# Optimization experiments

Hardware: AMD Instinct MI355X
Metric: run time of the kernel (lower is better)

Reference implementation:

```python
import jax, jax.numpy as jnp
import numpy as np

B = 262144
EDGES_SRC = np.array([0, 0, 0, 0])
EDGES_DST = np.array([1, 2, 3, 4])
PRED_IDS = np.array([[0, 10, 14], [1, 11, 18], [2, 12, 22], [3, 13, 26]])
O_IDS = np.array([0, 1, 2, 3, 10, 11, 12, 13, 14, 18, 22, 26])


def _xavier(k, shape):
    fan_out, fan_in = shape
    bound = float(np.sqrt(6.0 / (fan_in + fan_out)))
    return jax.random.uniform(k, shape, jnp.float32, -bound, bound)


def setup_inputs() -> dict:
    key = jax.random.key(0)
    ks = jax.random.split(key, 12)
    return {
        "initial_c": jax.random.uniform(ks[0], (B, 30), jnp.float32),
        "initial_s": jax.random.normal(ks[1], (B, 9), jnp.float32),
        "current_c": jax.random.uniform(ks[2], (B, 30), jnp.float32),
        "eps": jax.random.normal(ks[3], (B, 8), jnp.float32),
        # GnnMessagePassing params (torch Linear: y = x @ W.T + b)
        "W1": _xavier(ks[4], (128, 13)), "b1": jnp.zeros(128, jnp.float32),
        "W2": _xavier(ks[5], (39, 128)), "b2": jnp.zeros(39, jnp.float32),
        "W3": _xavier(ks[6], (128, 39)), "b3": jnp.zeros(128, jnp.float32),
        "Wm": _xavier(ks[7], (8, 128)), "bm": jnp.zeros(8, jnp.float32),
        "Wv": _xavier(ks[8], (8, 128)), "bv": jnp.zeros(8, jnp.float32),
        # Decoder params: [25 -> 32 -> 12], sigmoid output (binary=True)
        "Wd1": _xavier(ks[9], (32, 25)), "bd1": jnp.zeros(32, jnp.float32),
        "Wd2": _xavier(ks[10], (12, 32)), "bd2": jnp.zeros(12, jnp.float32),
    }


def reference(initial_c, initial_s, current_c, eps,
              W1, b1, W2, b2, W3, b3, Wm, bm, Wv, bv, Wd1, bd1, Wd2, bd2):
    bsz = current_c.shape[0]
    eye = jnp.eye(5, dtype=current_c.dtype)
    # per-edge constant one-hot pair features: [4, 10]
    edge_onehot = jnp.concatenate([eye[EDGES_SRC], eye[EDGES_DST]], axis=-1)
    edge_onehot = jnp.broadcast_to(edge_onehot[:, None, :], (4, bsz, 10))
    # gather predicate triplets per edge: [B, 4, 3] -> [4, B, 3]
    preds = jnp.transpose(current_c[:, PRED_IDS], (1, 0, 2))
    inp_mp = jnp.concatenate([edge_onehot, preds], axis=-1)  # [4, B, 13]

    # message MLP + sum over edge dim
    x = jax.nn.relu(jnp.einsum('ebi,oi->ebo', inp_mp, W1) + b1)  # [4, B, 128]
    x = jax.nn.relu(jnp.einsum('ebi,oi->ebo', x, W2) + b2)       # [4, B, 39]
    x = x.sum(axis=0)                                            # [B, 39]
    x = jax.nn.relu(x @ W3.T + b3)                               # [B, 128]
    means = x @ Wm.T + bm                                        # [B, 8]
    log_var = x @ Wv.T + bv                                      # [B, 8]

    # reparameterization
    z = eps * jnp.exp(0.5 * log_var) + means

    # decoder: [one-hot(node 0) | initial_c[o_ids] | z] -> sigmoid MLP
    node0 = jnp.broadcast_to(eye[0], (bsz, 5))
    inp_dec = jnp.concatenate([node0, initial_c[:, O_IDS], z], axis=1)  # [B, 25]
    h = jax.nn.relu(inp_dec @ Wd1.T + bd1)
    recon_x = jax.nn.sigmoid(h @ Wd2.T + bd2)  # [B, 12]
    return recon_x, means, log_var, z
```

## Files before the change

kernel.cpp:

```cpp
#include <hip/hip_runtime.h>
#include <hip/hip_bf16.h>

#define TPB 256
#define PREP_BLOCKS 64

typedef __attribute__((ext_vector_type(8))) short short8;
typedef __attribute__((ext_vector_type(4))) float f32x4;

#define G_W2F   0
#define G_MVF   12288
#define G_D1F   16384
#define G_D2F   18432
#define G_CEAB  19456
#define G_B2P   23552
#define G_B3    23744
#define G_BMV   24256
#define G_D1C   24320
#define G_BD2   24448
#define G_W3F   24512
#define G_END   40896

#define PW_SWC  0
#define PW_SIC  768
#define PW_ST   2048
#define PW_BUF  4352
#define PW_MH   8704
#define PW_SZ   9984
#define LDS_TOT (4 * PW_SZ)

__device__ __forceinline__ unsigned short f2bf(float f) {
    unsigned int u = __float_as_uint(f);
    unsigned int r = u + 0x7fffu + ((u >> 16) & 1u);
    return (unsigned short)(r >> 16);
}
__device__ __forceinline__ unsigned int pk(float a, float b) {
    __hip_bfloat162 h = __float22bfloat162_rn(make_float2(a, b));
    unsigned int u; __builtin_memcpy(&u, &h, 4); return u;
}
__device__ __forceinline__ unsigned short bfbits(float v) {
    return (unsigned short)(pk(v, v) & 0xffffu);
}

__global__ void prep_kernel(
    const float* __restrict__ W1, const float* __restrict__ b1,
    const float* __restrict__ W2, const float* __restrict__ b2,
    const float* __restrict__ W3, const float* __restrict__ b3,
    const float* __restrict__ Wm, const float* __restrict__ bm,
    const float* __restrict__ Wv, const float* __restrict__ bv,
    const float* __restrict__ Wd1, const float* __restrict__ bd1,
    const float* __restrict__ Wd2, const float* __restrict__ bd2,
    unsigned char* __restrict__ ws)
{
    const int g0 = blockIdx.x * TPB + threadIdx.x;
    const int gs = gridDim.x * TPB;
    unsigned short* w2f = (unsigned short*)(ws + G_W2F);
    for (int i = g0; i < 6144; i += gs) {
        int j = i & 7, lane = (i >> 3) & 63, ts = i >> 9;
        int tt = ts >> 2, s = ts & 3;
        int n = 16 * tt + (lane & 15), k = 32 * s + 8 * (lane >> 4) + j;
        w2f[i] = (n < 39) ? f2bf(W2[n * 128 + k]) : 0;
    }
    unsigned short* w3f = (unsigned short*)(ws + G_W3F);
    for (int i = g0; i < 8192; i += gs) {
        int j = i & 7, lane = (i >> 3) & 63, ns = i >> 9;
        int nt = ns >> 1, s = ns & 1;
        int n = 16 * nt + (lane & 15), k = 32 * s + 8 * (lane >> 4) + j;
        w3f[i] = (k < 39) ? f2bf(W3[n * 39 + k]) : 0;
    }
    unsigned short* mvf = (unsigned short*)(ws + G_MVF);
    for (int i = g0; i < 2048; i += gs) {
        int j = i & 7, lane = (i >> 3) & 63, s = i >> 9;
        int n = lane & 15, k = 32 * s + 8 * (lane >> 4) + j;
        mvf[i] = f2bf(n < 8 ? Wm[n * 128 + k] : Wv[(n - 8) * 128 + k]);
    }
    unsigned short* d1f = (unsigned short*)(ws + G_D1F);
    for (int i = g0; i < 1024; i += gs) {
        int j = i & 7, lane = (i >> 3) & 63, tt = i >> 9;
        int n = 16 * tt + (lane & 15), k = 8 * (lane >> 4) + j;
        d1f[i] = (k < 20) ? f2bf(Wd1[n * 25 + 5 + k]) : 0;
    }
    unsigned short* d2f = (unsigned short*)(ws + G_D2F);
    for (int i = g0; i < 512; i += gs) {
        int j = i & 7, lane = i >> 3;
        int n = lane & 15, k = 8 * (lane >> 4) + j;
        d2f[i] = (n < 12) ? f2bf(Wd2[n * 32 + k]) : 0;
    }
    unsigned short* ceab = (unsigned short*)(ws + G_CEAB);
    for (int i = g0; i < 2048; i += gs) {
        int c = i & 3, n = (i >> 2) & 127, e = i >> 9;
        float v = (c < 3) ? W1[n * 13 + 10 + c]
                          : (W1[n * 13 + 0] + W1[n * 13 + 6 + e] + b1[n]);
        ceab[i] = f2bf(v);
    }
    float* fb = (float*)(ws + G_B2P);
    for (int i = g0; i < 48; i += gs) fb[i] = (i < 39) ? b2[i] : 0.f;
    fb = (float*)(ws + G_B3);
    for (int i = g0; i < 128; i += gs) fb[i] = b3[i];
    fb = (float*)(ws + G_BMV);
    for (int i = g0; i < 16; i += gs) fb[i] = (i < 8) ? bm[i] : bv[i - 8];
    fb = (float*)(ws + G_D1C);
    for (int i = g0; i < 32; i += gs) fb[i] = Wd1[i * 25 + 0] + bd1[i];
    fb = (float*)(ws + G_BD2);
    for (int i = g0; i < 16; i += gs) fb[i] = (i < 12) ? bd2[i] : 0.f;
}

union S8 { short8 v; uint4 u; };

__global__ __launch_bounds__(TPB, 2) void vae_mfma(
    const float* __restrict__ ic, const float* __restrict__ cc,
    const float* __restrict__ eps,
    const unsigned char* __restrict__ ws,
    float* __restrict__ out, int B)
{
    __shared__ __attribute__((aligned(16))) unsigned char lds[LDS_TOT];
    const int tid = threadIdx.x;

    const int lane = tid & 63, w = tid >> 6;
    const int quad = lane >> 4, n16 = lane & 15;
    const bool q0 = (quad == 0);
    const long rb = ((long)blockIdx.x * 4 + w) * 16;
    unsigned char* pw = lds + w * PW_SZ;

    {
        int r = lane >> 2, g = lane & 3;
        long R = rb + r;
        const int cbase[4] = {0, 2, 10, 12};
        const int csing[4] = {14, 18, 22, 26};
        const float* crow = cc + R * 30;
        const float* irow = ic + R * 30;
        float2 cp = *(const float2*)(crow + cbase[g]);
        float  cs = crow[csing[g]];
        float2 ip = *(const float2*)(irow + cbase[g]);
        float  is = irow[csing[g]];
        float* swc = (float*)(pw + PW_SWC);
        *(float2*)(swc + r * 12 + 2 * g) = cp;
        swc[r * 12 + 8 + g] = cs;
        unsigned short* sic = (unsigned short*)(pw + PW_SIC);
        *(unsigned int*)(sic + r * 40 + 2 * g) = pk(ip.x, ip.y);
        sic[r * 40 + 8 + g] = bfbits(is);
        if (g < 3) *(unsigned long long*)(sic + r * 40 + 20 + 4 * g) = 0ull;
        unsigned short* st = (unsigned short*)(pw + PW_ST);
        *(unsigned long long*)(st + r * 72 + 48 + 4 * g) = 0ull;
    }

    short8 B2[12];
    #pragma unroll
    for (int ts = 0; ts < 12; ts++) {
        S8 x; x.u = *(const uint4*)(ws + G_W2F + (ts * 64 + lane) * 16);
        B2[ts] = x.v;
    }
    const float b2v0 = *(const float*)(ws + G_B2P + n16 * 4);
    const float b2v1 = *(const float*)(ws + G_B2P + (16 + n16) * 4);
    const float b2v2 = *(const float*)(ws + G_B2P + (32 + n16) * 4);

    float pa[4], pb[4], pc[4];
    {
        const float* swcr = (const float*)(pw + PW_SWC) + n16 * 12;
        float4 t0 = *(const float4*)(swcr);
        float4 t1 = *(const float4*)(swcr + 4);
        float4 t2 = *(const float4*)(swcr + 8);
        pa[0] = t0.x; pa[1] = t0.y; pa[2] = t0.z; pa[3] = t0.w;
        pb[0] = t1.x; pb[1] = t1.y; pb[2] = t1.z; pb[3] = t1.w;
        pc[0] = t2.x; pc[1] = t2.y; pc[2] = t2.z; pc[3] = t2.w;
    }

    f32x4 ss0 = {0,0,0,0}, ss1 = {0,0,0,0}, ss2 = {0,0,0,0};
    unsigned short* x1t = (unsigned short*)(pw + PW_BUF);

    #pragma unroll
    for (int e = 0; e < 4; e++) {
        S8 a1;
        a1.u.x = q0 ? pk(pa[e], pb[e]) : 0u;
        a1.u.y = q0 ? pk(pc[e], 1.0f) : 0u;
        a1.u.z = 0u; a1.u.w = 0u;
        const unsigned long long* cb =
            (const unsigned long long*)(ws + G_CEAB + e * 1024);
        f32x4 cr[8];
        #pragma unroll
        for (int nt = 0; nt < 8; nt++) {
            unsigned long long bw = cb[nt * 16 + n16];
            S8 bf;
            bf.u.x = q0 ? (unsigned int)bw : 0u;
            bf.u.y = q0 ? (unsigned int)(bw >> 32) : 0u;
            bf.u.z = 0u; bf.u.w = 0u;
            f32x4 z = {0, 0, 0, 0};
            cr[nt] = __builtin_amdgcn_mfma_f32_16x16x32_bf16(a1.v, bf.v, z, 0, 0, 0);
        }
        #pragma unroll
        for (int nt = 0; nt < 8; nt++) {
            #pragma unroll
            for (int r = 0; r < 4; r++)
                x1t[(quad * 4 + r) * 136 + nt * 16 + n16] = bfbits(fmaxf(cr[nt][r], 0.f));
        }
        f32x4 c0 = {b2v0, b2v0, b2v0, b2v0};
        f32x4 c1 = {b2v1, b2v1, b2v1, b2v1};
        f32x4 c2 = {b2v2, b2v2, b2v2, b2v2};
        #pragma unroll
        for (int s = 0; s < 4; s++) {
            S8 a2; a2.u = *(const uint4*)(x1t + n16 * 136 + s * 32 + quad * 8);
            c0 = __builtin_amdgcn_mfma_f32_16x16x32_bf16(a2.v, B2[s],     c0, 0, 0, 0);
            c1 = __builtin_amdgcn_mfma_f32_16x16x32_bf16(a2.v, B2[4 + s], c1, 0, 0, 0);
            c2 = __builtin_amdgcn_mfma_f32_16x16x32_bf16(a2.v, B2[8 + s], c2, 0, 0, 0);
        }
        #pragma unroll
        for (int r = 0; r < 4; r++) {
            ss0[r] += fmaxf(c0[r], 0.f);
            ss1[r] += fmaxf(c1[r], 0.f);
            ss2[r] += fmaxf(c2[r], 0.f);
        }
    }

    unsigned short* st = (unsigned short*)(pw + PW_ST);
    #pragma unroll
    for (int r = 0; r < 4; r++) {
        int row = quad * 4 + r;
        st[row * 72 + n16]      = bfbits(ss0[r]);
        st[row * 72 + 16 + n16] = bfbits(ss1[r]);
        st[row * 72 + 32 + n16] = bfbits(ss2[r]);
    }

    S8 A30, A31;
    A30.u = *(const uint4*)(st + n16 * 72 + quad * 8);
    A31.u = *(const uint4*)(st + n16 * 72 + 32 + quad * 8);
    const uint4* w3g = (const uint4*)(ws + G_W3F);
    unsigned short* x3t = (unsigned short*)(pw + PW_BUF);
    const float* b3p = (const float*)(ws + G_B3);
    #pragma unroll
    for (int nt = 0; nt < 8; nt++) {
        float bb = b3p[nt * 16 + n16];
        f32x4 c = {bb, bb, bb, bb};
        S8 bf0, bf1;
        bf0.u = w3g[(nt * 2 + 0) * 64 + lane];
        bf1.u = w3g[(nt * 2 + 1) * 64 + lane];
        c = __builtin_amdgcn_mfma_f32_16x16x32_bf16(A30.v, bf0.v, c, 0, 0, 0);
        c = __builtin_amdgcn_mfma_f32_16x16x32_bf16(A31.v, bf1.v, c, 0, 0, 0);
        #pragma unroll
        for (int r = 0; r < 4; r++)
            x3t[(quad * 4 + r) * 136 + nt * 16 + n16] = bfbits(fmaxf(c[r], 0.f));
    }

    S8 Ah0, Ah1, Ah2, Ah3;
    Ah0.u = *(const uint4*)(x3t + n16 * 136 + 0  + quad * 8);
    Ah1.u = *(const uint4*)(x3t + n16 * 136 + 32 + quad * 8);
    Ah2.u = *(const uint4*)(x3t + n16 * 136 + 64 + quad * 8);
    Ah3.u = *(const uint4*)(x3t + n16 * 136 + 96 + quad * 8);
    float bmvv = *(const float*)(ws + G_BMV + n16 * 4);
    f32x4 cm = {bmvv, bmvv, bmvv, bmvv};
    {
        S8 bm0; bm0.u = *(const uint4*)(ws + G_MVF + (0 * 64 + lane) * 16);
        cm = __builtin_amdgcn_mfma_f32_16x16x32_bf16(Ah0.v, bm0.v, cm, 0, 0, 0);
        S8 bm1; bm1.u = *(const uint4*)(ws + G_MVF + (1 * 64 + lane) * 16);
        cm = __builtin_amdgcn_mfma_f32_16x16x32_bf16(Ah1.v, bm1.v, cm, 0, 0, 0);
        S8 bm2; bm2.u = *(const uint4*)(ws + G_MVF + (2 * 64 + lane) * 16);
        cm = __builtin_amdgcn_mfma_f32_16x16x32_bf16(Ah2.v, bm2.v, cm, 0, 0, 0);
        S8 bm3; bm3.u = *(const uint4*)(ws + G_MVF + (3 * 64 + lane) * 16);
        cm = __builtin_amdgcn_mfma_f32_16x16x32_bf16(Ah3.v, bm3.v, cm, 0, 0, 0);
    }
    float* mlv = (float*)(pw + PW_MH);
    #pragma unroll
    for (int r = 0; r < 4; r++) mlv[(quad * 4 + r) * 18 + n16] = cm[r];

    {
        int r = lane >> 2, g = lane & 3;
        long R = rb + r;
        const float* mrow = mlv + r * 18;
        float2 mn = *(const float2*)(mrow + 2 * g);
        float2 lv = *(const float2*)(mrow + 8 + 2 * g);
        float2 ev = *(const float2*)(eps + R * 8 + 2 * g);
        float z0 = fmaf(ev.x, __expf(0.5f * lv.x), mn.x);
        float z1 = fmaf(ev.y, __expf(0.5f * lv.y), mn.y);
        *(float2*)(out + (long)B * 12 + R * 8 + 2 * g) = mn;
        *(float2*)(out + (long)B * 20 + R * 8 + 2 * g) = lv;
        *(float2*)(out + (long)B * 28 + R * 8 + 2 * g) = make_float2(z0, z1);
        unsigned short* sic = (unsigned short*)(pw + PW_SIC);
        *(unsigned int*)(sic + r * 40 + 12 + 2 * g) = pk(z0, z1);
    }

    S8 Ad;
    Ad.u = *(const uint4*)((const unsigned short*)(pw + PW_SIC) + n16 * 40 + quad * 8);
    unsigned short* ht = (unsigned short*)(pw + PW_MH);
    #pragma unroll
    for (int t = 0; t < 2; t++) {
        float dc = *(const float*)(ws + G_D1C + (t * 16 + n16) * 4);
        f32x4 c = {dc, dc, dc, dc};
        S8 bd; bd.u = *(const uint4*)(ws + G_D1F + (t * 64 + lane) * 16);
        c = __builtin_amdgcn_mfma_f32_16x16x32_bf16(Ad.v, bd.v, c, 0, 0, 0);
        #pragma unroll
        for (int r = 0; r < 4; r++)
            ht[(quad * 4 + r) * 40 + t * 16 + n16] = bfbits(fmaxf(c[r], 0.f));
    }

    S8 Ah2d; Ah2d.u = *(const uint4*)(ht + n16 * 40 + quad * 8);
    float bd2v = *(const float*)(ws + G_BD2 + n16 * 4);
    f32x4 cr2 = {bd2v, bd2v, bd2v, bd2v};
    S8 b2d; b2d.u = *(const uint4*)(ws + G_D2F + lane * 16);
    cr2 = __builtin_amdgcn_mfma_f32_16x16x32_bf16(Ah2d.v, b2d.v, cr2, 0, 0, 0);
    if (n16 < 12) {
        #pragma unroll
        for (int r = 0; r < 4; r++)
            out[(rb + quad * 4 + r) * 12 + n16] = 1.f / (1.f + __expf(-cr2[r]));
    }
}

extern "C" void kernel_launch(void* const* d_in, const int* in_sizes, int n_in,
                              void* d_out, int out_size, void* d_ws, size_t ws_size,
                              hipStream_t stream) {
    const float* ic  = (const float*)d_in[0];
    const float* cc  = (const float*)d_in[2];
    const float* eps = (const float*)d_in[3];

    const int B = in_sizes[3] / 8;
    const int nblocks = B / 64;

    prep_kernel<<<PREP_BLOCKS, TPB, 0, stream>>>(
        (const float*)d_in[4],  (const float*)d_in[5],
        (const float*)d_in[6],  (const float*)d_in[7],
        (const float*)d_in[8],  (const float*)d_in[9],
        (const float*)d_in[10], (const float*)d_in[11],
        (const float*)d_in[12], (const float*)d_in[13],
        (const float*)d_in[14], (const float*)d_in[15],
        (const float*)d_in[16], (const float*)d_in[17],
        (unsigned char*)d_ws);
    vae_mfma<<<nblocks, TPB, 0, stream>>>(
        ic, cc, eps, (const unsigned char*)d_ws, (float*)d_out, B);
}
```

Before: 191.8 us.

## Chain MFMA layers in registers via transposed products and permuted weight K order

Swaps operand roles so each layer computes the transposed product, with weights as A and activations as B. Weight K indices are permuted in the prep kernel so one layer's accumulator output feeds the next layer's B fragment directly in registers. This removes all LDS staging, LDS round trips and the shared memory allocation. Lane exchanges for log_var and z use ds_bpermute, and outputs are written as float4 per lane. The risk is more register pressure and a fragile permutation mapping.

```diff
diff --git a/kernel.cpp b/kernel.cpp
--- a/kernel.cpp
+++ b/kernel.cpp
@@ -20,14 +20,6 @@
 #define G_W3F   24512
 #define G_END   40896
 
-#define PW_SWC  0
-#define PW_SIC  768
-#define PW_ST   2048
-#define PW_BUF  4352
-#define PW_MH   8704
-#define PW_SZ   9984
-#define LDS_TOT (4 * PW_SZ)
-
 __device__ __forceinline__ unsigned short f2bf(float f) {
     unsigned int u = __float_as_uint(f);
     unsigned int r = u + 0x7fffu + ((u >> 16) & 1u);
@@ -36,9 +28,6 @@
 __device__ __forceinline__ unsigned int pk(float a, float b) {
     __hip_bfloat162 h = __float22bfloat162_rn(make_float2(a, b));
     unsigned int u; __builtin_memcpy(&u, &h, 4); return u;
-}
-__device__ __forceinline__ unsigned short bfbits(float v) {
-    return (unsigned short)(pk(v, v) & 0xffffu);
 }
 
 __global__ void prep_kernel(
@@ -56,34 +45,39 @@
     unsigned short* w2f = (unsigned short*)(ws + G_W2F);
     for (int i = g0; i < 6144; i += gs) {
         int j = i & 7, lane = (i >> 3) & 63, ts = i >> 9;
-        int tt = ts >> 2, s = ts & 3;
-        int n = 16 * tt + (lane & 15), k = 32 * s + 8 * (lane >> 4) + j;
-        w2f[i] = (n < 39) ? f2bf(W2[n * 128 + k]) : 0;
+        int t = ts >> 2, s = ts & 3, q = lane >> 4;
+        int n = 16 * t + (lane & 15);
+        int phys = 16 * (2 * s + (j >> 2)) + 4 * q + (j & 3);
+        w2f[i] = (n < 39) ? f2bf(W2[n * 128 + phys]) : 0;
     }
     unsigned short* w3f = (unsigned short*)(ws + G_W3F);
     for (int i = g0; i < 8192; i += gs) {
         int j = i & 7, lane = (i >> 3) & 63, ns = i >> 9;
-        int nt = ns >> 1, s = ns & 1;
-        int n = 16 * nt + (lane & 15), k = 32 * s + 8 * (lane >> 4) + j;
-        w3f[i] = (k < 39) ? f2bf(W3[n * 39 + k]) : 0;
+        int nt = ns >> 1, s = ns & 1, q = lane >> 4;
+        int n = 16 * nt + (lane & 15);
+        int phys = 16 * (2 * s + (j >> 2)) + 4 * q + (j & 3);
+        w3f[i] = (phys < 39) ? f2bf(W3[n * 39 + phys]) : 0;
     }
     unsigned short* mvf = (unsigned short*)(ws + G_MVF);
     for (int i = g0; i < 2048; i += gs) {
         int j = i & 7, lane = (i >> 3) & 63, s = i >> 9;
-        int n = lane & 15, k = 32 * s + 8 * (lane >> 4) + j;
-        mvf[i] = f2bf(n < 8 ? Wm[n * 128 + k] : Wv[(n - 8) * 128 + k]);
+        int q = lane >> 4, n = lane & 15;
+        int phys = 16 * (2 * s + (j >> 2)) + 4 * q + (j & 3);
+        mvf[i] = f2bf(n < 8 ? Wm[n * 128 + phys] : Wv[(n - 8) * 128 + phys]);
     }
     unsigned short* d1f = (unsigned short*)(ws + G_D1F);
     for (int i = g0; i < 1024; i += gs) {
         int j = i & 7, lane = (i >> 3) & 63, tt = i >> 9;
-        int n = 16 * tt + (lane & 15), k = 8 * (lane >> 4) + j;
-        d1f[i] = (k < 20) ? f2bf(Wd1[n * 25 + 5 + k]) : 0;
+        int q = lane >> 4, n = 16 * tt + (lane & 15);
+        int phys = 16 * (j >> 2) + 4 * q + (j & 3);
+        d1f[i] = (phys < 20) ? f2bf(Wd1[n * 25 + 5 + phys]) : 0;
     }
     unsigned short* d2f = (unsigned short*)(ws + G_D2F);
     for (int i = g0; i < 512; i += gs) {
         int j = i & 7, lane = i >> 3;
-        int n = lane & 15, k = 8 * (lane >> 4) + j;
-        d2f[i] = (n < 12) ? f2bf(Wd2[n * 32 + k]) : 0;
+        int q = lane >> 4, n = lane & 15;
+        int phys = 16 * (j >> 2) + 4 * q + (j & 3);
+        d2f[i] = (n < 12) ? f2bf(Wd2[n * 32 + phys]) : 0;
     }
     unsigned short* ceab = (unsigned short*)(ws + G_CEAB);
     for (int i = g0; i < 2048; i += gs) {
@@ -106,101 +100,74 @@
 
 union S8 { short8 v; uint4 u; };
 
+#define MFMA(a, b, c) __builtin_amdgcn_mfma_f32_16x16x32_bf16(a, b, c, 0, 0, 0)
+
 __global__ __launch_bounds__(TPB, 2) void vae_mfma(
     const float* __restrict__ ic, const float* __restrict__ cc,
     const float* __restrict__ eps,
     const unsigned char* __restrict__ ws,
     float* __restrict__ out, int B)
 {
-    __shared__ __attribute__((aligned(16))) unsigned char lds[LDS_TOT];
     const int tid = threadIdx.x;
-
     const int lane = tid & 63, w = tid >> 6;
     const int quad = lane >> 4, n16 = lane & 15;
     const bool q0 = (quad == 0);
     const long rb = ((long)blockIdx.x * 4 + w) * 16;
-    unsigned char* pw = lds + w * PW_SZ;
-
-    {
-        int r = lane >> 2, g = lane & 3;
-        long R = rb + r;
-        const int cbase[4] = {0, 2, 10, 12};
-        const int csing[4] = {14, 18, 22, 26};
-        const float* crow = cc + R * 30;
-        const float* irow = ic + R * 30;
-        float2 cp = *(const float2*)(crow + cbase[g]);
-        float  cs = crow[csing[g]];
-        float2 ip = *(const float2*)(irow + cbase[g]);
-        float  is = irow[csing[g]];
-        float* swc = (float*)(pw + PW_SWC);
-        *(float2*)(swc + r * 12 + 2 * g) = cp;
-        swc[r * 12 + 8 + g] = cs;
-        unsigned short* sic = (unsigned short*)(pw + PW_SIC);
-        *(unsigned int*)(sic + r * 40 + 2 * g) = pk(ip.x, ip.y);
-        sic[r * 40 + 8 + g] = bfbits(is);
-        if (g < 3) *(unsigned long long*)(sic + r * 40 + 20 + 4 * g) = 0ull;
-        unsigned short* st = (unsigned short*)(pw + PW_ST);
-        *(unsigned long long*)(st + r * 72 + 48 + 4 * g) = 0ull;
-    }
-
-    short8 B2[12];
-    #pragma unroll
-    for (int ts = 0; ts < 12; ts++) {
-        S8 x; x.u = *(const uint4*)(ws + G_W2F + (ts * 64 + lane) * 16);
-        B2[ts] = x.v;
-    }
-    const float b2v0 = *(const float*)(ws + G_B2P + n16 * 4);
-    const float b2v1 = *(const float*)(ws + G_B2P + (16 + n16) * 4);
-    const float b2v2 = *(const float*)(ws + G_B2P + (32 + n16) * 4);
-
-    float pa[4], pb[4], pc[4];
-    {
-        const float* swcr = (const float*)(pw + PW_SWC) + n16 * 12;
-        float4 t0 = *(const float4*)(swcr);
-        float4 t1 = *(const float4*)(swcr + 4);
-        float4 t2 = *(const float4*)(swcr + 8);
-        pa[0] = t0.x; pa[1] = t0.y; pa[2] = t0.z; pa[3] = t0.w;
-        pb[0] = t1.x; pb[1] = t1.y; pb[2] = t1.z; pb[3] = t1.w;
-        pc[0] = t2.x; pc[1] = t2.y; pc[2] = t2.z; pc[3] = t2.w;
-    }
+    const long Rl = rb + n16;
+
+    float pa[4] = {0,0,0,0}, pb[4] = {0,0,0,0}, pc[4] = {0,0,0,0};
+    if (q0) {
+        const float* crow = cc + Rl * 30;
+        float2 t0 = *(const float2*)(crow);
+        float2 t1 = *(const float2*)(crow + 2);
+        float2 t2 = *(const float2*)(crow + 10);
+        float2 t3 = *(const float2*)(crow + 12);
+        pa[0] = t0.x; pa[1] = t0.y; pa[2] = t1.x; pa[3] = t1.y;
+        pb[0] = t2.x; pb[1] = t2.y; pb[2] = t3.x; pb[3] = t3.y;
+        pc[0] = crow[14]; pc[1] = crow[18]; pc[2] = crow[22]; pc[3] = crow[26];
+    }
+
+    S8 W2F[12];
+    #pragma unroll
+    for (int ts = 0; ts < 12; ts++)
+        W2F[ts].u = *(const uint4*)(ws + G_W2F + (ts * 64 + lane) * 16);
+    const float* b2p = (const float*)(ws + G_B2P);
+    f32x4 b2q[3];
+    #pragma unroll
+    for (int t = 0; t < 3; t++)
+        b2q[t] = *(const f32x4*)(b2p + 16 * t + 4 * quad);
 
     f32x4 ss0 = {0,0,0,0}, ss1 = {0,0,0,0}, ss2 = {0,0,0,0};
-    unsigned short* x1t = (unsigned short*)(pw + PW_BUF);
 
     #pragma unroll
     for (int e = 0; e < 4; e++) {
-        S8 a1;
-        a1.u.x = q0 ? pk(pa[e], pb[e]) : 0u;
-        a1.u.y = q0 ? pk(pc[e], 1.0f) : 0u;
-        a1.u.z = 0u; a1.u.w = 0u;
+        S8 bp;
+        bp.u.x = q0 ? pk(pa[e], pb[e]) : 0u;
+        bp.u.y = q0 ? pk(pc[e], 1.0f) : 0u;
+        bp.u.z = 0u; bp.u.w = 0u;
         const unsigned long long* cb =
             (const unsigned long long*)(ws + G_CEAB + e * 1024);
-        f32x4 cr[8];
+        S8 xf[4];
         #pragma unroll
-        for (int nt = 0; nt < 8; nt++) {
-            unsigned long long bw = cb[nt * 16 + n16];
-            S8 bf;
-            bf.u.x = q0 ? (unsigned int)bw : 0u;
-            bf.u.y = q0 ? (unsigned int)(bw >> 32) : 0u;
-            bf.u.z = 0u; bf.u.w = 0u;
-            f32x4 z = {0, 0, 0, 0};
-            cr[nt] = __builtin_amdgcn_mfma_f32_16x16x32_bf16(a1.v, bf.v, z, 0, 0, 0);
+        for (int mt = 0; mt < 8; mt++) {
+            unsigned long long bw = cb[mt * 16 + n16];
+            S8 af;
+            af.u.x = q0 ? (unsigned int)bw : 0u;
+            af.u.y = q0 ? (unsigned int)(bw >> 32) : 0u;
+            af.u.z = 0u; af.u.w = 0u;
+            f32x4 z4 = {0,0,0,0};
+            f32x4 cr = MFMA(af.v, bp.v, z4);
+            unsigned int lo = pk(fmaxf(cr[0], 0.f), fmaxf(cr[1], 0.f));
+            unsigned int hi = pk(fmaxf(cr[2], 0.f), fmaxf(cr[3], 0.f));
+            if ((mt & 1) == 0) { xf[mt >> 1].u.x = lo; xf[mt >> 1].u.y = hi; }
+            else               { xf[mt >> 1].u.z = lo; xf[mt >> 1].u.w = hi; }
         }
-        #pragma unroll
-        for (int nt = 0; nt < 8; nt++) {
-            #pragma unroll
-            for (int r = 0; r < 4; r++)
-                x1t[(quad * 4 + r) * 136 + nt * 16 + n16] = bfbits(fmaxf(cr[nt][r], 0.f));
-        }
-        f32x4 c0 = {b2v0, b2v0, b2v0, b2v0};
-        f32x4 c1 = {b2v1, b2v1, b2v1, b2v1};
-        f32x4 c2 = {b2v2, b2v2, b2v2, b2v2};
+        f32x4 c0 = b2q[0], c1 = b2q[1], c2 = b2q[2];
         #pragma unroll
         for (int s = 0; s < 4; s++) {
-            S8 a2; a2.u = *(const uint4*)(x1t + n16 * 136 + s * 32 + quad * 8);
-            c0 = __builtin_amdgcn_mfma_f32_16x16x32_bf16(a2.v, B2[s],     c0, 0, 0, 0);
-            c1 = __builtin_amdgcn_mfma_f32_16x16x32_bf16(a2.v, B2[4 + s], c1, 0, 0, 0);
-            c2 = __builtin_amdgcn_mfma_f32_16x16x32_bf16(a2.v, B2[8 + s], c2, 0, 0, 0);
+            c0 = MFMA(W2F[s].v,     xf[s].v, c0);
+            c1 = MFMA(W2F[4 + s].v, xf[s].v, c1);
+            c2 = MFMA(W2F[8 + s].v, xf[s].v, c2);
         }
         #pragma unroll
         for (int r = 0; r < 4; r++) {
@@ -210,95 +177,100 @@
         }
     }
 
-    unsigned short* st = (unsigned short*)(pw + PW_ST);
-    #pragma unroll
-    for (int r = 0; r < 4; r++) {
-        int row = quad * 4 + r;
-        st[row * 72 + n16]      = bfbits(ss0[r]);
-        st[row * 72 + 16 + n16] = bfbits(ss1[r]);
-        st[row * 72 + 32 + n16] = bfbits(ss2[r]);
-    }
-
-    S8 A30, A31;
-    A30.u = *(const uint4*)(st + n16 * 72 + quad * 8);
-    A31.u = *(const uint4*)(st + n16 * 72 + 32 + quad * 8);
+    S8 sf0, sf1;
+    sf0.u.x = pk(ss0[0], ss0[1]); sf0.u.y = pk(ss0[2], ss0[3]);
+    sf0.u.z = pk(ss1[0], ss1[1]); sf0.u.w = pk(ss1[2], ss1[3]);
+    sf1.u.x = pk(ss2[0], ss2[1]); sf1.u.y = pk(ss2[2], ss2[3]);
+    sf1.u.z = 0u; sf1.u.w = 0u;
+
     const uint4* w3g = (const uint4*)(ws + G_W3F);
-    unsigned short* x3t = (unsigned short*)(pw + PW_BUF);
     const float* b3p = (const float*)(ws + G_B3);
+    S8 hf[4];
     #pragma unroll
     for (int nt = 0; nt < 8; nt++) {
-        float bb = b3p[nt * 16 + n16];
-        f32x4 c = {bb, bb, bb, bb};
-        S8 bf0, bf1;
-        bf0.u = w3g[(nt * 2 + 0) * 64 + lane];
-        bf1.u = w3g[(nt * 2 + 1) * 64 + lane];
-        c = __builtin_amdgcn_mfma_f32_16x16x32_bf16(A30.v, bf0.v, c, 0, 0, 0);
-        c = __builtin_amdgcn_mfma_f32_16x16x32_bf16(A31.v, bf1.v, c, 0, 0, 0);
-        #pragma unroll
-        for (int r = 0; r < 4; r++)
-            x3t[(quad * 4 + r) * 136 + nt * 16 + n16] = bfbits(fmaxf(c[r], 0.f));
-    }
-
-    S8 Ah0, Ah1, Ah2, Ah3;
-    Ah0.u = *(const uint4*)(x3t + n16 * 136 + 0  + quad * 8);
-    Ah1.u = *(const uint4*)(x3t + n16 * 136 + 32 + quad * 8);
-    Ah2.u = *(const uint4*)(x3t + n16 * 136 + 64 + quad * 8);
-    Ah3.u = *(const uint4*)(x3t + n16 * 136 + 96 + quad * 8);
-    float bmvv = *(const float*)(ws + G_BMV + n16 * 4);
-    f32x4 cm = {bmvv, bmvv, bmvv, bmvv};
-    {
-        S8 bm0; bm0.u = *(const uint4*)(ws + G_MVF + (0 * 64 + lane) * 16);
-        cm = __builtin_amdgcn_mfma_f32_16x16x32_bf16(Ah0.v, bm0.v, cm, 0, 0, 0);
-        S8 bm1; bm1.u = *(const uint4*)(ws + G_MVF + (1 * 64 + lane) * 16);
-        cm = __builtin_amdgcn_mfma_f32_16x16x32_bf16(Ah1.v, bm1.v, cm, 0, 0, 0);
-        S8 bm2; bm2.u = *(const uint4*)(ws + G_MVF + (2 * 64 + lane) * 16);
-        cm = __builtin_amdgcn_mfma_f32_16x16x32_bf16(Ah2.v, bm2.v, cm, 0, 0, 0);
-        S8 bm3; bm3.u = *(const uint4*)(ws + G_MVF + (3 * 64 + lane) * 16);
-        cm = __builtin_amdgcn_mfma_f32_16x16x32_bf16(Ah3.v, bm3.v, cm, 0, 0, 0);
-    }
-    float* mlv = (float*)(pw + PW_MH);
-    #pragma unroll
-    for (int r = 0; r < 4; r++) mlv[(quad * 4 + r) * 18 + n16] = cm[r];
-
-    {
-        int r = lane >> 2, g = lane & 3;
-        long R = rb + r;
-        const float* mrow = mlv + r * 18;
-        float2 mn = *(const float2*)(mrow + 2 * g);
-        float2 lv = *(const float2*)(mrow + 8 + 2 * g);
-        float2 ev = *(const float2*)(eps + R * 8 + 2 * g);
-        float z0 = fmaf(ev.x, __expf(0.5f * lv.x), mn.x);
-        float z1 = fmaf(ev.y, __expf(0.5f * lv.y), mn.y);
-        *(float2*)(out + (long)B * 12 + R * 8 + 2 * g) = mn;
-        *(float2*)(out + (long)B * 20 + R * 8 + 2 * g) = lv;
-        *(float2*)(out + (long)B * 28 + R * 8 + 2 * g) = make_float2(z0, z1);
-        unsigned short* sic = (unsigned short*)(pw + PW_SIC);
-        *(unsigned int*)(sic + r * 40 + 12 + 2 * g) = pk(z0, z1);
-    }
-
-    S8 Ad;
-    Ad.u = *(const uint4*)((const unsigned short*)(pw + PW_SIC) + n16 * 40 + quad * 8);
-    unsigned short* ht = (unsigned short*)(pw + PW_MH);
-    #pragma unroll
-    for (int t = 0; t < 2; t++) {
-        float dc = *(const float*)(ws + G_D1C + (t * 16 + n16) * 4);
-        f32x4 c = {dc, dc, dc, dc};
-        S8 bd; bd.u = *(const uint4*)(ws + G_D1F + (t * 64 + lane) * 16);
-        c = __builtin_amdgcn_mfma_f32_16x16x32_bf16(Ad.v, bd.v, c, 0, 0, 0);
-        #pragma unroll
-        for (int r = 0; r < 4; r++)
-            ht[(quad * 4 + r) * 40 + t * 16 + n16] = bfbits(fmaxf(c[r], 0.f));
-    }
-
-    S8 Ah2d; Ah2d.u = *(const uint4*)(ht + n16 * 40 + quad * 8);
-    float bd2v = *(const float*)(ws + G_BD2 + n16 * 4);
-    f32x4 cr2 = {bd2v, bd2v, bd2v, bd2v};
-    S8 b2d; b2d.u = *(const uint4*)(ws + G_D2F + lane * 16);
-    cr2 = __builtin_amdgcn_mfma_f32_16x16x32_bf16(Ah2d.v, b2d.v, cr2, 0, 0, 0);
-    if (n16 < 12) {
-        #pragma unroll
-        for (int r = 0; r < 4; r++)
-            out[(rb + quad * 4 + r) * 12 + n16] = 1.f / (1.f + __expf(-cr2[r]));
+        f32x4 c = *(const f32x4*)(b3p + nt * 16 + 4 * quad);
+        S8 a0, a1;
+        a0.u = w3g[(nt * 2 + 0) * 64 + lane];
+        a1.u = w3g[(nt * 2 + 1) * 64 + lane];
+        c = MFMA(a0.v, sf0.v, c);
+        c = MFMA(a1.v, sf1.v, c);
+        unsigned int lo = pk(fmaxf(c[0], 0.f), fmaxf(c[1], 0.f));
+        unsigned int hi = pk(fmaxf(c[2], 0.f), fmaxf(c[3], 0.f));
+        if ((nt & 1) == 0) { hf[nt >> 1].u.x = lo; hf[nt >> 1].u.y = hi; }
+        else               { hf[nt >> 1].u.z = lo; hf[nt >> 1].u.w = hi; }
+    }
+
+    f32x4 cm = *(const f32x4*)((const float*)(ws + G_BMV) + 4 * quad);
+    #pragma unroll
+    for (int s = 0; s < 4; s++) {
+        S8 a; a.u = *(const uint4*)(ws + G_MVF + (s * 64 + lane) * 16);
+        cm = MFMA(a.v, hf[s].v, cm);
+    }
+
+    const int addrLv = ((lane + 32) & 63) << 2;
+    float lvv[4];
+    #pragma unroll
+    for (int r = 0; r < 4; r++)
+        lvv[r] = __int_as_float(
+            __builtin_amdgcn_ds_bpermute(addrLv, __float_as_int(cm[r])));
+    float4 ev = *(const float4*)(eps + Rl * 8 + 4 * (quad & 1));
+    f32x4 zz;
+    zz[0] = fmaf(ev.x, __expf(0.5f * lvv[0]), cm[0]);
+    zz[1] = fmaf(ev.y, __expf(0.5f * lvv[1]), cm[1]);
+    zz[2] = fmaf(ev.z, __expf(0.5f * lvv[2]), cm[2]);
+    zz[3] = fmaf(ev.w, __expf(0.5f * lvv[3]), cm[3]);
+    float* pml = (float*)((quad < 2) ? (out + (long)B * 12) : (out + (long)B * 20));
+    *(float4*)(pml + Rl * 8 + 4 * (quad & 1)) = *(float4*)&cm;
+    if (quad < 2)
+        *(float4*)(out + (long)B * 28 + Rl * 8 + 4 * quad) = *(float4*)&zz;
+
+    const int addrZ = (n16 + (q0 ? 16 : 0)) << 2;
+    float zr[4];
+    #pragma unroll
+    for (int r = 0; r < 4; r++)
+        zr[r] = __int_as_float(
+            __builtin_amdgcn_ds_bpermute(addrZ, __float_as_int(zz[r])));
+
+    const float* irow = ic + Rl * 30;
+    float d0, d1, d2, d3;
+    if (quad == 3)      { d0 = zr[0];    d1 = zr[1];    d2 = zr[2];    d3 = zr[3]; }
+    else if (quad == 2) { d0 = irow[14]; d1 = irow[18]; d2 = irow[22]; d3 = irow[26]; }
+    else {
+        const float* p = irow + (quad ? 10 : 0);
+        float2 u0 = *(const float2*)(p);
+        float2 u1 = *(const float2*)(p + 2);
+        d0 = u0.x; d1 = u0.y; d2 = u1.x; d3 = u1.y;
+    }
+    S8 df;
+    df.u.x = pk(d0, d1);
+    df.u.y = pk(d2, d3);
+    df.u.z = q0 ? pk(zr[0], zr[1]) : 0u;
+    df.u.w = q0 ? pk(zr[2], zr[3]) : 0u;
+
+    const float* d1c = (const float*)(ws + G_D1C);
+    S8 a;
+    f32x4 ct = *(const f32x4*)(d1c + 4 * quad);
+    a.u = *(const uint4*)(ws + G_D1F + (0 * 64 + lane) * 16);
+    f32x4 h0 = MFMA(a.v, df.v, ct);
+    ct = *(const f32x4*)(d1c + 16 + 4 * quad);
+    a.u = *(const uint4*)(ws + G_D1F + (1 * 64 + lane) * 16);
+    f32x4 h1 = MFMA(a.v, df.v, ct);
+    S8 hf2;
+    hf2.u.x = pk(fmaxf(h0[0], 0.f), fmaxf(h0[1], 0.f));
+    hf2.u.y = pk(fmaxf(h0[2], 0.f), fmaxf(h0[3], 0.f));
+    hf2.u.z = pk(fmaxf(h1[0], 0.f), fmaxf(h1[1], 0.f));
+    hf2.u.w = pk(fmaxf(h1[2], 0.f), fmaxf(h1[3], 0.f));
+
+    f32x4 c2 = *(const f32x4*)((const float*)(ws + G_BD2) + 4 * quad);
+    S8 a2; a2.u = *(const uint4*)(ws + G_D2F + lane * 16);
+    c2 = MFMA(a2.v, hf2.v, c2);
+    if (quad < 3) {
+        float4 o;
+        o.x = 1.f / (1.f + __expf(-c2[0]));
+        o.y = 1.f / (1.f + __expf(-c2[1]));
+        o.z = 1.f / (1.f + __expf(-c2[2]));
+        o.w = 1.f / (1.f + __expf(-c2[3]));
+        *(float4*)(out + Rl * 12 + 4 * quad) = o;
     }
 }
 
```

Measured after the change: 199.2 us. 1.04x slower.
